# Optimization experiments

Measured on AMD Instinct MI355X. Metric: run time of the kernel, lower is better.

Reference implementation:

```python
import jax, jax.numpy as jnp
import numpy as np

S, B, E = 2048, 2, 768
H = 12
D = E // H  # 64
SCALE = D ** -0.5


def setup_inputs() -> dict:
    key = jax.random.key(0)
    ks = jax.random.split(key, 10)
    inp = {
        "query": jax.random.normal(ks[0], (S, B, E), dtype=jnp.float32),
        "attn_bias": jax.random.normal(ks[1], (B * H, S, S), dtype=jnp.float32) * 0.1,
        "key_padding_mask": jax.random.randint(ks[2], (B, S), 0, 2).astype(bool),
        "Wq": jax.random.normal(ks[3], (E, E), dtype=jnp.float32) * (E ** -0.5),
        "bq": jnp.zeros((E,), dtype=jnp.float32),
        "Wk": jax.random.normal(ks[4], (E, E), dtype=jnp.float32) * (E ** -0.5),
        "bk": jnp.zeros((E,), dtype=jnp.float32),
        "Wv": jax.random.normal(ks[5], (E, E), dtype=jnp.float32) * (E ** -0.5),
        "bv": jnp.zeros((E,), dtype=jnp.float32),
        "Wo": jax.random.normal(ks[6], (E, E), dtype=jnp.float32) * (E ** -0.5),
        "bo": jnp.zeros((E,), dtype=jnp.float32),
    }
    return inp


def reference(query, attn_bias, key_padding_mask, Wq, bq, Wk, bk, Wv, bv, Wo, bo):
    s, b, e = query.shape
    # projections (torch Linear: x @ W.T + b)
    q = (query @ Wq.T + bq) * SCALE
    k = query @ Wk.T + bk
    v = query @ Wv.T + bv
    # [s, b, e] -> [b*h, s, d]
    def to_heads(x):
        return x.reshape(s, b * H, D).transpose(1, 0, 2)
    q, k, v = to_heads(q), to_heads(k), to_heads(v)
    # scores [b*h, s_q, s_k]
    scores = jnp.einsum('nqd,nkd->nqk', q, k) + attn_bias
    # key padding mask: [b, s_k] -> broadcast over heads and queries
    scores = scores.reshape(b, H, s, s)
    scores = jnp.where(key_padding_mask[:, None, None, :], -jnp.inf, scores)
    scores = scores.reshape(b * H, s, s)
    probs = jax.nn.softmax(scores, axis=-1)
    attn = jnp.einsum('nqk,nkd->nqd', probs, v)  # [b*h, s, d]
    attn = attn.transpose(1, 0, 2).reshape(s, b, e)
    return attn @ Wo.T + bo
```

## Files before the change

kernel.cpp:

```cpp
#include <hip/hip_runtime.h>
#include <hip/hip_bf16.h>

typedef __attribute__((ext_vector_type(8))) short s16x8;
typedef __attribute__((ext_vector_type(4))) float f32x4;
typedef unsigned short u16;
typedef unsigned int u32;

#define SDIM 2048
#define BDIM 2
#define HDIM 12
#define DDIM 64
#define EDIM 768
#define MDIM 4096
#define SCALE_Q 0.125f
#define KSPLIT 1024
#define NIT (KSPLIT / 32)
#define HFRAG 131072

static __device__ __forceinline__ f32x4 zero4() {
    f32x4 v; v[0] = v[1] = v[2] = v[3] = 0.f; return v;
}

static __device__ __forceinline__ u16 f2b(float x) {
    u32 u = __builtin_bit_cast(u32, x);
    u32 lsb = (u >> 16) & 1u;
    u += 0x7fffu + lsb;
    return (u16)(u >> 16);
}

static __device__ __forceinline__ u32 cvt_pk_bf16(float lo, float hi) {
    u32 r;
    asm("v_cvt_pk_bf16_f32 %0, %1, %2" : "=v"(r) : "v"(lo), "v"(hi));
    return r;
}

static __device__ __forceinline__ f32x4 mfma16(s16x8 a, s16x8 b, f32x4 c) {
    return __builtin_amdgcn_mfma_f32_16x16x32_bf16(a, b, c, 0, 0, 0);
}

static __device__ __forceinline__ void gload_lds16(const void* g, void* l) {
    __builtin_amdgcn_global_load_lds(
        (const __attribute__((address_space(1))) void*)g,
        (__attribute__((address_space(3))) void*)l, 16, 0, 0);
}

__global__ void mask_bits_kernel(const u32* __restrict__ raw, u32* __restrict__ outbits) {
    __shared__ int okInt, okFloat;
    int t = threadIdx.x;
    if (t == 0) { okInt = 1; okFloat = 1; }
    __syncthreads();
    int li = 1, lf = 1;
    for (int i = t; i < 1024; i += blockDim.x) {
        u32 v = raw[i];
        if (v > 1u) li = 0;
        if (v != 0u && v != 0x3F800000u) lf = 0;
    }
    if (!li) atomicAnd(&okInt, 0);
    if (!lf) atomicAnd(&okFloat, 0);
    __syncthreads();
    const unsigned char* rb = (const unsigned char*)raw;
    if (t < (BDIM * SDIM) / 32) {
        u32 bits = 0;
        for (int j = 0; j < 32; ++j) {
            int i = t * 32 + j;
            int v;
            if (okInt)        v = (int)raw[i];
            else if (okFloat) v = (raw[i] != 0u) ? 1 : 0;
            else              v = (int)rb[i];
            bits |= (v ? 1u : 0u) << j;
        }
        outbits[t] = bits;
    }
}

__global__ __launch_bounds__(256) void conv_f32_bf16(
    const float* __restrict__ s, u16* __restrict__ d, int n8)
{
    int i = blockIdx.x * 256 + threadIdx.x;
    if (i >= n8) return;
    float4 x0 = ((const float4*)s)[(size_t)i * 2];
    float4 x1 = ((const float4*)s)[(size_t)i * 2 + 1];
    uint4 o;
    o.x = (u32)f2b(x0.x) | ((u32)f2b(x0.y) << 16);
    o.y = (u32)f2b(x0.z) | ((u32)f2b(x0.w) << 16);
    o.z = (u32)f2b(x1.x) | ((u32)f2b(x1.y) << 16);
    o.w = (u32)f2b(x1.z) | ((u32)f2b(x1.w) << 16);
    ((uint4*)d)[i] = o;
}

__global__ __launch_bounds__(256) void gemm_qkv(
    const u16* __restrict__ A,
    const u16* __restrict__ wq, const u16* __restrict__ wk, const u16* __restrict__ wv,
    const float* __restrict__ bq, const float* __restrict__ bk, const float* __restrict__ bv,
    u16* __restrict__ qout, u16* __restrict__ kout, u16* __restrict__ vout)
{
    __shared__ u16 Al[64 * 56];
    __shared__ u16 Bl[64 * 56];
    int tid = threadIdx.x;
    int lane = tid & 63, w = tid >> 6;
    int r16 = lane & 15, g4 = lane >> 4;
    int wm = w >> 1, wn = w & 1;
    int mb = blockIdx.x * 64;
    int nbg = blockIdx.y * 64;
    int mid = nbg / EDIM;
    int nb = nbg - mid * EDIM;
    const u16* W = (mid == 0) ? wq : (mid == 1) ? wk : wv;
    const float* bias = (mid == 0) ? bq : (mid == 1) ? bk : bv;
    float scale = (mid == 0) ? SCALE_Q : 1.0f;

    f32x4 acc[2][2];
    acc[0][0] = zero4(); acc[0][1] = zero4(); acc[1][0] = zero4(); acc[1][1] = zero4();

    int srow = tid >> 2, scol = (tid & 3) * 8;

    for (int kb = 0; kb < EDIM; kb += 32) {
        __syncthreads();
        *(uint4*)&Al[srow * 56 + scol] =
            *(const uint4*)&A[(size_t)(mb + srow) * EDIM + kb + scol];
        *(uint4*)&Bl[srow * 56 + scol] =
            *(const uint4*)&W[(size_t)(nb + srow) * EDIM + kb + scol];
        __syncthreads();
        s16x8 a[2], bb[2];
        #pragma unroll
        for (int mi = 0; mi < 2; ++mi)
            a[mi] = *(const s16x8*)&Al[(wm * 32 + mi * 16 + r16) * 56 + g4 * 8];
        #pragma unroll
        for (int ni = 0; ni < 2; ++ni)
            bb[ni] = *(const s16x8*)&Bl[(wn * 32 + ni * 16 + r16) * 56 + g4 * 8];
        #pragma unroll
        for (int mi = 0; mi < 2; ++mi)
            #pragma unroll
            for (int ni = 0; ni < 2; ++ni)
                acc[mi][ni] = mfma16(a[mi], bb[ni], acc[mi][ni]);
    }

    #pragma unroll
    for (int mi = 0; mi < 2; ++mi) {
        #pragma unroll
        for (int ni = 0; ni < 2; ++ni) {
            int n = nb + wn * 32 + ni * 16 + r16;
            float bv_ = bias[n];
            #pragma unroll
            for (int r = 0; r < 4; ++r) {
                int m = mb + wm * 32 + mi * 16 + g4 * 4 + r;
                float c = (acc[mi][ni][r] + bv_) * scale;
                int s_ = m >> 1, b_ = m & 1, h_ = n >> 6, d_ = n & 63;
                if (mid == 0) {
                    qout[((size_t)(b_ * HDIM + h_) * SDIM + s_) * DDIM + d_] = f2b(c);
                } else if (mid == 1) {
                    size_t p = (size_t)(b_ * HDIM + h_) * HFRAG
                             + (size_t)(s_ >> 4) * 1024 + (size_t)((d_ >> 5) & 1) * 512
                             + (size_t)(((d_ >> 3) & 3) * 16 + (s_ & 15)) * 8 + (d_ & 7);
                    kout[p] = f2b(c);
                } else {
                    size_t p = (size_t)(b_ * HDIM + h_) * HFRAG
                             + (size_t)(s_ >> 5) * 2048 + (size_t)((d_ >> 4) & 3) * 512
                             + (size_t)(((s_ >> 3) & 3) * 16 + (d_ & 15)) * 8 + (s_ & 7);
                    vout[p] = f2b(c);
                }
            }
        }
    }
}

__global__ __launch_bounds__(256) void gemm_out(
    const u16* __restrict__ A, const u16* __restrict__ Wb,
    const float* __restrict__ bias, float* __restrict__ out_rm)
{
    __shared__ u16 Al[64 * 56];
    __shared__ u16 Bl[64 * 56];
    int tid = threadIdx.x;
    int lane = tid & 63, w = tid >> 6;
    int r16 = lane & 15, g4 = lane >> 4;
    int wm = w >> 1, wn = w & 1;
    int mb = blockIdx.x * 64, nb = blockIdx.y * 64;

    f32x4 acc[2][2];
    acc[0][0] = zero4(); acc[0][1] = zero4(); acc[1][0] = zero4(); acc[1][1] = zero4();

    int srow = tid >> 2, scol = (tid & 3) * 8;

    for (int kb = 0; kb < EDIM; kb += 32) {
        __syncthreads();
        *(uint4*)&Al[srow * 56 + scol] =
            *(const uint4*)&A[(size_t)(mb + srow) * EDIM + kb + scol];
        *(uint4*)&Bl[srow * 56 + scol] =
            *(const uint4*)&Wb[(size_t)(nb + srow) * EDIM + kb + scol];
        __syncthreads();
        s16x8 a[2], bb[2];
        #pragma unroll
        for (int mi = 0; mi < 2; ++mi)
            a[mi] = *(const s16x8*)&Al[(wm * 32 + mi * 16 + r16) * 56 + g4 * 8];
        #pragma unroll
        for (int ni = 0; ni < 2; ++ni)
            bb[ni] = *(const s16x8*)&Bl[(wn * 32 + ni * 16 + r16) * 56 + g4 * 8];
        #pragma unroll
        for (int mi = 0; mi < 2; ++mi)
            #pragma unroll
            for (int ni = 0; ni < 2; ++ni)
                acc[mi][ni] = mfma16(a[mi], bb[ni], acc[mi][ni]);
    }

    #pragma unroll
    for (int mi = 0; mi < 2; ++mi) {
        #pragma unroll
        for (int ni = 0; ni < 2; ++ni) {
            int n = nb + wn * 32 + ni * 16 + r16;
            float bv_ = bias[n];
            #pragma unroll
            for (int r = 0; r < 4; ++r) {
                int m = mb + wm * 32 + mi * 16 + g4 * 4 + r;
                out_rm[(size_t)m * EDIM + n] = acc[mi][ni][r] + bv_;
            }
        }
    }
}

struct KV { s16x8 k0, k1, k2, k3, v0, v1, v2, v3; u32 mw; };

__global__ __launch_bounds__(128) void attn_fused(
    const u16* __restrict__ qw, const u16* __restrict__ kf_g,
    const u16* __restrict__ vf_g, const float* __restrict__ bias,
    const u32* __restrict__ maskBits, u16* __restrict__ attn_out)
{
    __shared__ __align__(1024) unsigned char SM[24576];

    int flat = blockIdx.y * 64 + blockIdx.x;
    int virt = (flat & 7) * 192 + (flat >> 3);
    int qt = virt & 63, bh = virt >> 6;

    int tid = threadIdx.x;
    int w = tid >> 6, lane = tid & 63;
    int r16 = lane & 15, g4 = lane >> 4;
    int ga = g4 >> 1, gb = g4 & 1;
    int qbase = qt * 32;
    int b_ = bh / HDIM, h_ = bh % HDIM;
    const u16* Q  = qw   + (size_t)bh * SDIM * DDIM;
    const u16* KF = kf_g + (size_t)bh * HFRAG;
    const u16* VF = vf_g + (size_t)bh * HFRAG;
    const float* BrowQ = bias + (size_t)bh * SDIM * SDIM + (size_t)qbase * SDIM;
    const u32* mB = maskBits + b_ * (SDIM / 32);

    unsigned char* wb = SM + w * 12288;
    float* RingW = (float*)wb;

    int srcLo = (2 * gb) * 16 + r16;
    int srcHi = (2 * gb + 1) * 16 + r16;

    s16x8 qf[2][2];
    #pragma unroll
    for (int h = 0; h < 2; ++h) {
        qf[h][0] = *(const s16x8*)&Q[(size_t)(qbase + 16 * h + r16) * DDIM + g4 * 8];
        qf[h][1] = *(const s16x8*)&Q[(size_t)(qbase + 16 * h + r16) * DDIM + g4 * 8 + 32];
    }

    f32x4 accO[2][4];
    #pragma unroll
    for (int h = 0; h < 2; ++h)
        #pragma unroll
        for (int dt = 0; dt < 4; ++dt) accO[h][dt] = zero4();
    float m_run[2] = {-1e30f, -1e30f}, l_run[2] = {0.f, 0.f};

    const int k0 = w * KSPLIT;

    auto issue_kv = [&](int t, KV& dst) {
        int tc = t < NIT ? t : NIT - 1;
        int kbn = k0 + tc * 32;
        const u16* KT = KF + (size_t)(kbn >> 4) * 1024;
        dst.k0 = *(const s16x8*)&KT[lane * 8];
        dst.k1 = *(const s16x8*)&KT[512 + lane * 8];
        dst.k2 = *(const s16x8*)&KT[1024 + lane * 8];
        dst.k3 = *(const s16x8*)&KT[1536 + lane * 8];
        const u16* VT = VF + (size_t)(kbn >> 5) * 2048;
        dst.v0 = *(const s16x8*)&VT[lane * 8];
        dst.v1 = *(const s16x8*)&VT[512 + lane * 8];
        dst.v2 = *(const s16x8*)&VT[1024 + lane * 8];
        dst.v3 = *(const s16x8*)&VT[1536 + lane * 8];
        dst.mw = mB[kbn >> 5];
    };

    auto stage_bias = [&](int t) {
        int tc = t < NIT ? t : NIT - 1;
        int kb = k0 + tc * 32;
        unsigned char* slot = wb + (tc % 3) * 4096;
        int sq = (lane & 7) ^ ((lane >> 3) & 7);
        #pragma unroll
        for (int j = 0; j < 4; ++j) {
            int row = j * 8 + (lane >> 3);
            gload_lds16(&BrowQ[(size_t)row * SDIM + kb + sq * 4], slot + j * 1024);
        }
    };

    auto compute = [&](int t, KV& cur) {
        u32 mw = cur.mw;
        const float* Bs = RingW + (t % 3) * 1024;
        f32x4 sc[2][2];
        #pragma unroll
        for (int h = 0; h < 2; ++h) {
            sc[h][0] = mfma16(cur.k1, qf[h][1], mfma16(cur.k0, qf[h][0], zero4()));
            sc[h][1] = mfma16(cur.k3, qf[h][1], mfma16(cur.k2, qf[h][0], zero4()));
        }
        #pragma unroll
        for (int h = 0; h < 2; ++h) {
            int rr = 16 * h + r16;
            #pragma unroll
            for (int kt = 0; kt < 2; ++kt) {
                float4 bc = *(const float4*)&Bs[rr * 32 + (((4 * kt + g4) ^ (r16 & 7)) * 4)];
                u32 mseg = (mw >> (16 * kt + 4 * g4)) & 0xF;
                sc[h][kt][0] = (mseg & 1) ? -1e30f : sc[h][kt][0] + bc.x;
                sc[h][kt][1] = (mseg & 2) ? -1e30f : sc[h][kt][1] + bc.y;
                sc[h][kt][2] = (mseg & 4) ? -1e30f : sc[h][kt][2] + bc.z;
                sc[h][kt][3] = (mseg & 8) ? -1e30f : sc[h][kt][3] + bc.w;
            }
        }
        #pragma unroll
        for (int h = 0; h < 2; ++h) {
            float pm = fmaxf(
                fmaxf(fmaxf(sc[h][0][0], sc[h][0][1]), fmaxf(sc[h][0][2], sc[h][0][3])),
                fmaxf(fmaxf(sc[h][1][0], sc[h][1][1]), fmaxf(sc[h][1][2], sc[h][1][3])));
            pm = fmaxf(pm, __shfl_xor(pm, 16));
            pm = fmaxf(pm, __shfl_xor(pm, 32));
            bool norescale = __all(pm <= m_run[h] + 4.f);
            float mn = norescale ? m_run[h] : fmaxf(m_run[h], pm);
            float p[8];
            #pragma unroll
            for (int kt = 0; kt < 2; ++kt)
                #pragma unroll
                for (int r = 0; r < 4; ++r)
                    p[kt * 4 + r] = __expf(sc[h][kt][r] - mn);
            float ps = ((p[0] + p[1]) + (p[2] + p[3])) + ((p[4] + p[5]) + (p[6] + p[7]));
            ps += __shfl_xor(ps, 16);
            ps += __shfl_xor(ps, 32);
            if (norescale) {
                l_run[h] += ps;
            } else {
                float alpha = __expf(m_run[h] - mn);
                l_run[h] = l_run[h] * alpha + ps;
                m_run[h] = mn;
                float aR0 = __shfl(alpha, g4 * 4 + 0);
                float aR1 = __shfl(alpha, g4 * 4 + 1);
                float aR2 = __shfl(alpha, g4 * 4 + 2);
                float aR3 = __shfl(alpha, g4 * 4 + 3);
                #pragma unroll
                for (int dt = 0; dt < 4; ++dt) {
                    accO[h][dt][0] *= aR0;
                    accO[h][dt][1] *= aR1;
                    accO[h][dt][2] *= aR2;
                    accO[h][dt][3] *= aR3;
                }
            }
            u32 W0 = cvt_pk_bf16(p[0], p[1]);
            u32 W1 = cvt_pk_bf16(p[2], p[3]);
            u32 W2 = cvt_pk_bf16(p[4], p[5]);
            u32 W3 = cvt_pk_bf16(p[6], p[7]);
            u32 o0A = (u32)__shfl((int)W0, srcLo), o0B = (u32)__shfl((int)W2, srcLo);
            u32 o1A = (u32)__shfl((int)W1, srcLo), o1B = (u32)__shfl((int)W3, srcLo);
            u32 o2A = (u32)__shfl((int)W0, srcHi), o2B = (u32)__shfl((int)W2, srcHi);
            u32 o3A = (u32)__shfl((int)W1, srcHi), o3B = (u32)__shfl((int)W3, srcHi);
            uint4 pw;
            pw.x = ga ? o0B : o0A;
            pw.y = ga ? o1B : o1A;
            pw.z = ga ? o2B : o2A;
            pw.w = ga ? o3B : o3A;
            s16x8 pf = __builtin_bit_cast(s16x8, pw);
            accO[h][0] = mfma16(pf, cur.v0, accO[h][0]);
            accO[h][1] = mfma16(pf, cur.v1, accO[h][1]);
            accO[h][2] = mfma16(pf, cur.v2, accO[h][2]);
            accO[h][3] = mfma16(pf, cur.v3, accO[h][3]);
        }
    };

    KV A, B;
    issue_kv(0, A);
    stage_bias(0);
    stage_bias(1);

    for (int t = 0; t < NIT; t += 2) {
        issue_kv(t + 1, B);
        stage_bias(t + 2);
        asm volatile("s_waitcnt vmcnt(17)" ::: "memory");
        __builtin_amdgcn_sched_barrier(0);
        compute(t, A);

        issue_kv(t + 2, A);
        stage_bias(t + 3);
        asm volatile("s_waitcnt vmcnt(17)" ::: "memory");
        __builtin_amdgcn_sched_barrier(0);
        compute(t + 1, B);
    }

    __syncthreads();
    float* As = (float*)SM;
    float* Ml = (float*)(SM + 17408);
    float* Ll = Ml + 64;
    #pragma unroll
    for (int h = 0; h < 2; ++h)
        #pragma unroll
        for (int dt = 0; dt < 4; ++dt)
            #pragma unroll
            for (int r = 0; r < 4; ++r)
                As[(size_t)(w * 32 + 16 * h + g4 * 4 + r) * 68 + dt * 16 + r16] = accO[h][dt][r];
    if (g4 == 0) {
        #pragma unroll
        for (int h = 0; h < 2; ++h) {
            Ml[w * 32 + 16 * h + r16] = m_run[h];
            Ll[w * 32 + 16 * h + r16] = l_run[h];
        }
    }
    __syncthreads();

    #pragma unroll
    for (int h = 0; h < 2; ++h) {
        #pragma unroll
        for (int dg = 0; dg < 2; ++dg) {
            int d = w * 32 + dg * 16 + r16;
            #pragma unroll
            for (int r = 0; r < 4; ++r) {
                int q = 16 * h + g4 * 4 + r;
                float m0 = Ml[q], m1 = Ml[32 + q];
                float mt = fmaxf(m0, m1);
                float e0 = __expf(m0 - mt), e1 = __expf(m1 - mt);
                float lt = Ll[q] * e0 + Ll[32 + q] * e1;
                float o = (As[(size_t)q * 68 + d] * e0 + As[(size_t)(32 + q) * 68 + d] * e1) / lt;
                attn_out[((size_t)(qbase + q) * BDIM + b_) * EDIM + h_ * DDIM + d] = f2b(o);
            }
        }
    }
}

extern "C" void kernel_launch(void* const* d_in, const int* in_sizes, int n_in,
                              void* d_out, int out_size, void* d_ws, size_t ws_size,
                              hipStream_t stream) {
    const float* query     = (const float*)d_in[0];
    const float* attn_bias = (const float*)d_in[1];
    const u32*   mask_raw  = (const u32*)d_in[2];
    const float* Wq = (const float*)d_in[3];
    const float* bq = (const float*)d_in[4];
    const float* Wk = (const float*)d_in[5];
    const float* bk = (const float*)d_in[6];
    const float* Wv = (const float*)d_in[7];
    const float* bv = (const float*)d_in[8];
    const float* Wo = (const float*)d_in[9];
    const float* bo = (const float*)d_in[10];
    float* out = (float*)d_out;

    char* ws = (char*)d_ws;
    u32* maskB = (u32*)ws;
    const size_t HEADSZ = (size_t)BDIM * HDIM * SDIM * DDIM;
    const size_t WSZ = (size_t)EDIM * EDIM;
    u16* qws = (u16*)(ws + 16384);
    u16* kws = qws + HEADSZ;
    u16* vws = kws + HEADSZ;
    u16* aws = vws + HEADSZ;
    u16* qbf = aws;
    u16* wWq = aws + HEADSZ;
    u16* wWk = wWq + WSZ;
    u16* wWv = wWk + WSZ;
    u16* wWo = wWv + WSZ;

    mask_bits_kernel<<<1, 256, 0, stream>>>(mask_raw, maskB);

    conv_f32_bf16<<<(int)(MDIM * EDIM / 8 / 256), 256, 0, stream>>>(query, qbf, MDIM * EDIM / 8);
    conv_f32_bf16<<<(int)(WSZ / 8 / 256), 256, 0, stream>>>(Wq, wWq, (int)(WSZ / 8));
    conv_f32_bf16<<<(int)(WSZ / 8 / 256), 256, 0, stream>>>(Wk, wWk, (int)(WSZ / 8));
    conv_f32_bf16<<<(int)(WSZ / 8 / 256), 256, 0, stream>>>(Wv, wWv, (int)(WSZ / 8));
    conv_f32_bf16<<<(int)(WSZ / 8 / 256), 256, 0, stream>>>(Wo, wWo, (int)(WSZ / 8));

    dim3 gq(MDIM / 64, (3 * EDIM) / 64);
    gemm_qkv<<<gq, 256, 0, stream>>>(qbf, wWq, wWk, wWv, bq, bk, bv, qws, kws, vws);

    dim3 ga(64, BDIM * HDIM);
    attn_fused<<<ga, 128, 0, stream>>>(qws, kws, vws, attn_bias, maskB, aws);

    dim3 go(MDIM / 64, EDIM / 64);
    gemm_out<<<go, 256, 0, stream>>>(aws, wWo, bo, out);
}
```

Baseline: 223.0 us.

## Split attention keys across four waves and batch weight conversions into one launch

Measured after the change: 389.7 us. +74.7%, slower.

```diff
diff --git a/kernel.cpp b/kernel.cpp
--- a/kernel.cpp
+++ b/kernel.cpp
@@ -13,7 +13,7 @@
 #define EDIM 768
 #define MDIM 4096
 #define SCALE_Q 0.125f
-#define KSPLIT 1024
+#define KSPLIT 512
 #define NIT (KSPLIT / 32)
 #define HFRAG 131072
 
@@ -76,6 +76,27 @@
 __global__ __launch_bounds__(256) void conv_f32_bf16(
     const float* __restrict__ s, u16* __restrict__ d, int n8)
 {
+    int i = blockIdx.x * 256 + threadIdx.x;
+    if (i >= n8) return;
+    float4 x0 = ((const float4*)s)[(size_t)i * 2];
+    float4 x1 = ((const float4*)s)[(size_t)i * 2 + 1];
+    uint4 o;
+    o.x = (u32)f2b(x0.x) | ((u32)f2b(x0.y) << 16);
+    o.y = (u32)f2b(x0.z) | ((u32)f2b(x0.w) << 16);
+    o.z = (u32)f2b(x1.x) | ((u32)f2b(x1.y) << 16);
+    o.w = (u32)f2b(x1.z) | ((u32)f2b(x1.w) << 16);
+    ((uint4*)d)[i] = o;
+}
+
+__global__ __launch_bounds__(256) void conv4_w(
+    const float* __restrict__ w0, const float* __restrict__ w1,
+    const float* __restrict__ w2, const float* __restrict__ w3,
+    u16* __restrict__ d0, u16* __restrict__ d1,
+    u16* __restrict__ d2, u16* __restrict__ d3, int n8)
+{
+    int m = blockIdx.y;
+    const float* s = (m == 0) ? w0 : (m == 1) ? w1 : (m == 2) ? w2 : w3;
+    u16* d = (m == 0) ? d0 : (m == 1) ? d1 : (m == 2) ? d2 : d3;
     int i = blockIdx.x * 256 + threadIdx.x;
     if (i >= n8) return;
     float4 x0 = ((const float4*)s)[(size_t)i * 2];
@@ -218,12 +239,12 @@
 
 struct KV { s16x8 k0, k1, k2, k3, v0, v1, v2, v3; u32 mw; };
 
-__global__ __launch_bounds__(128) void attn_fused(
+__global__ __launch_bounds__(256, 4) void attn_fused(
     const u16* __restrict__ qw, const u16* __restrict__ kf_g,
     const u16* __restrict__ vf_g, const float* __restrict__ bias,
     const u32* __restrict__ maskBits, u16* __restrict__ attn_out)
 {
-    __shared__ __align__(1024) unsigned char SM[24576];
+    __shared__ __align__(1024) unsigned char SM[35840];
 
     int flat = blockIdx.y * 64 + blockIdx.x;
     int virt = (flat & 7) * 192 + (flat >> 3);
@@ -241,7 +262,7 @@
     const float* BrowQ = bias + (size_t)bh * SDIM * SDIM + (size_t)qbase * SDIM;
     const u32* mB = maskBits + b_ * (SDIM / 32);
 
-    unsigned char* wb = SM + w * 12288;
+    unsigned char* wb = SM + w * 8192;
     float* RingW = (float*)wb;
 
     int srcLo = (2 * gb) * 16 + r16;
@@ -282,7 +303,7 @@
     auto stage_bias = [&](int t) {
         int tc = t < NIT ? t : NIT - 1;
         int kb = k0 + tc * 32;
-        unsigned char* slot = wb + (tc % 3) * 4096;
+        unsigned char* slot = wb + (t & 1) * 4096;
         int sq = (lane & 7) ^ ((lane >> 3) & 7);
         #pragma unroll
         for (int j = 0; j < 4; ++j) {
@@ -293,7 +314,7 @@
 
     auto compute = [&](int t, KV& cur) {
         u32 mw = cur.mw;
-        const float* Bs = RingW + (t % 3) * 1024;
+        const float* Bs = RingW + (t & 1) * 1024;
         f32x4 sc[2][2];
         #pragma unroll
         for (int h = 0; h < 2; ++h) {
@@ -373,26 +394,25 @@
     KV A, B;
     issue_kv(0, A);
     stage_bias(0);
-    stage_bias(1);
 
     for (int t = 0; t < NIT; t += 2) {
         issue_kv(t + 1, B);
-        stage_bias(t + 2);
-        asm volatile("s_waitcnt vmcnt(17)" ::: "memory");
+        stage_bias(t + 1);
+        asm volatile("s_waitcnt vmcnt(13)" ::: "memory");
         __builtin_amdgcn_sched_barrier(0);
         compute(t, A);
 
         issue_kv(t + 2, A);
-        stage_bias(t + 3);
-        asm volatile("s_waitcnt vmcnt(17)" ::: "memory");
+        stage_bias(t + 2);
+        asm volatile("s_waitcnt vmcnt(13)" ::: "memory");
         __builtin_amdgcn_sched_barrier(0);
         compute(t + 1, B);
     }
 
     __syncthreads();
     float* As = (float*)SM;
-    float* Ml = (float*)(SM + 17408);
-    float* Ll = Ml + 64;
+    float* Ml = (float*)(SM + 34816);
+    float* Ll = Ml + 128;
     #pragma unroll
     for (int h = 0; h < 2; ++h)
         #pragma unroll
@@ -409,22 +429,26 @@
     }
     __syncthreads();
 
-    #pragma unroll
-    for (int h = 0; h < 2; ++h) {
-        #pragma unroll
-        for (int dg = 0; dg < 2; ++dg) {
-            int d = w * 32 + dg * 16 + r16;
-            #pragma unroll
-            for (int r = 0; r < 4; ++r) {
-                int q = 16 * h + g4 * 4 + r;
-                float m0 = Ml[q], m1 = Ml[32 + q];
-                float mt = fmaxf(m0, m1);
-                float e0 = __expf(m0 - mt), e1 = __expf(m1 - mt);
-                float lt = Ll[q] * e0 + Ll[32 + q] * e1;
-                float o = (As[(size_t)q * 68 + d] * e0 + As[(size_t)(32 + q) * 68 + d] * e1) / lt;
-                attn_out[((size_t)(qbase + q) * BDIM + b_) * EDIM + h_ * DDIM + d] = f2b(o);
-            }
-        }
+    {
+        int q = tid >> 3, d0q = (tid & 7) * 8;
+        float m0 = Ml[q], m1 = Ml[32 + q], m2 = Ml[64 + q], m3 = Ml[96 + q];
+        float mt = fmaxf(fmaxf(m0, m1), fmaxf(m2, m3));
+        float e0 = __expf(m0 - mt), e1 = __expf(m1 - mt);
+        float e2 = __expf(m2 - mt), e3 = __expf(m3 - mt);
+        float lt = Ll[q] * e0 + Ll[32 + q] * e1 + Ll[64 + q] * e2 + Ll[96 + q] * e3;
+        float inv = 1.0f / lt;
+        u16 ob[8];
+        #pragma unroll
+        for (int j = 0; j < 8; ++j) {
+            int d = d0q + j;
+            float o = (As[(size_t)q * 68 + d] * e0
+                     + As[(size_t)(32 + q) * 68 + d] * e1
+                     + As[(size_t)(64 + q) * 68 + d] * e2
+                     + As[(size_t)(96 + q) * 68 + d] * e3) * inv;
+            ob[j] = f2b(o);
+        }
+        *(uint4*)&attn_out[((size_t)(qbase + q) * BDIM + b_) * EDIM + h_ * DDIM + d0q] =
+            *(const uint4*)ob;
     }
 }
 
@@ -461,16 +485,14 @@
     mask_bits_kernel<<<1, 256, 0, stream>>>(mask_raw, maskB);
 
     conv_f32_bf16<<<(int)(MDIM * EDIM / 8 / 256), 256, 0, stream>>>(query, qbf, MDIM * EDIM / 8);
-    conv_f32_bf16<<<(int)(WSZ / 8 / 256), 256, 0, stream>>>(Wq, wWq, (int)(WSZ / 8));
-    conv_f32_bf16<<<(int)(WSZ / 8 / 256), 256, 0, stream>>>(Wk, wWk, (int)(WSZ / 8));
-    conv_f32_bf16<<<(int)(WSZ / 8 / 256), 256, 0, stream>>>(Wv, wWv, (int)(WSZ / 8));
-    conv_f32_bf16<<<(int)(WSZ / 8 / 256), 256, 0, stream>>>(Wo, wWo, (int)(WSZ / 8));
+    dim3 gc((int)(WSZ / 8 / 256), 4);
+    conv4_w<<<gc, 256, 0, stream>>>(Wq, Wk, Wv, Wo, wWq, wWk, wWv, wWo, (int)(WSZ / 8));
 
     dim3 gq(MDIM / 64, (3 * EDIM) / 64);
     gemm_qkv<<<gq, 256, 0, stream>>>(qbf, wWq, wWk, wWv, bq, bk, bv, qws, kws, vws);
 
     dim3 ga(64, BDIM * HDIM);
-    attn_fused<<<ga, 128, 0, stream>>>(qws, kws, vws, attn_bias, maskB, aws);
+    attn_fused<<<ga, 256, 0, stream>>>(qws, kws, vws, attn_bias, maskB, aws);
 
     dim3 go(MDIM / 64, EDIM / 64);
     gemm_out<<<go, 256, 0, stream>>>(aws, wWo, bo, out);
```
